# Performance work log

Hardware: AMD Instinct MI355X
Metric: run time of the kernel (lower is better)

Reference implementation:

```python
import jax, jax.numpy as jnp
import numpy as np

B, S, H = 2, 2048, 1024
NH, HD = 16, 64  # num heads, head dim
EPS = 1e-12


def setup_inputs() -> dict:
    key = jax.random.key(0)
    ks = jax.random.split(key, 10)
    sc = 1.0 / np.sqrt(H)
    return {
        "hidden_states": jax.random.normal(ks[0], (B, S, H), jnp.float32),
        "Wq": jax.random.normal(ks[1], (H, H), jnp.float32) * sc,
        "bq": jnp.zeros((H,), jnp.float32),
        "Wk": jax.random.normal(ks[2], (H, H), jnp.float32) * sc,
        "bk": jnp.zeros((H,), jnp.float32),
        "Wv": jax.random.normal(ks[3], (H, H), jnp.float32) * sc,
        "bv": jnp.zeros((H,), jnp.float32),
        "Wo": jax.random.normal(ks[4], (H, H), jnp.float32) * sc,
        "bo": jnp.zeros((H,), jnp.float32),
        "ln_g": jnp.ones((H,), jnp.float32),
        "ln_b": jnp.zeros((H,), jnp.float32),
    }


def reference(hidden_states, Wq, bq, Wk, bk, Wv, bv, Wo, bo, ln_g, ln_b):
    x = hidden_states  # [B,S,H]
    def split_heads(t):
        return t.reshape(B, S, NH, HD).transpose(0, 2, 1, 3)  # [B,NH,S,HD]
    q = split_heads(x @ Wq.T + bq)
    k = split_heads(x @ Wk.T + bk)
    v = split_heads(x @ Wv.T + bv)
    scores = jnp.einsum("bhqd,bhkd->bhqk", q, k) / np.sqrt(HD)
    causal = jnp.tril(jnp.ones((S, S), bool))  # [S,S]
    scores = jnp.where(causal[None, None], scores, -jnp.inf)
    probs = jax.nn.softmax(scores, axis=-1)
    ctx = jnp.einsum("bhqk,bhkd->bhqd", probs, v)
    ctx = ctx.transpose(0, 2, 1, 3).reshape(B, S, H)
    attn_out = ctx @ Wo.T + bo
    y = attn_out + x
    mu = jnp.mean(y, axis=-1, keepdims=True)
    var = jnp.mean((y - mu) ** 2, axis=-1, keepdims=True)
    return (y - mu) / jnp.sqrt(var + EPS) * ln_g + ln_b
```

## Files before the change

### kernel.cpp

```cpp
#include <hip/hip_runtime.h>

#define B_  2
#define S_  2048
#define H_  1024
#define NH_ 16
#define HD_ 64
#define M_  (B_*S_)

typedef __attribute__((ext_vector_type(8))) __bf16 bf16x8;
typedef __attribute__((ext_vector_type(4))) float  f32x4;
typedef __attribute__((ext_vector_type(8))) unsigned short us8;
typedef __attribute__((ext_vector_type(4))) float  fl4;

__device__ __forceinline__ unsigned short f2bf(float f) {
    unsigned int u = __float_as_uint(f);
    u += 0x7fffu + ((u >> 16) & 1u);
    return (unsigned short)(u >> 16);
}

__global__ __launch_bounds__(256) void cast_kernel(
    const float* __restrict__ x,
    const float* __restrict__ wq, const float* __restrict__ wk,
    const float* __restrict__ wv, const float* __restrict__ wo,
    unsigned short* __restrict__ xb, unsigned short* __restrict__ wb) {
    size_t t  = (size_t)blockIdx.x * 256 + threadIdx.x;
    size_t e0 = t * 4;
    const size_t XN = (size_t)M_ * H_;
    const float* src;
    unsigned short* dst;
    if (e0 < XN) { src = x + e0; dst = xb + e0; }
    else {
        size_t j = e0 - XN;
        int w = (int)(j >> 20);
        size_t off = j & ((1u << 20) - 1);
        const float* wp = (w == 0) ? wq : (w == 1) ? wk : (w == 2) ? wv : wo;
        src = wp + off; dst = wb + j;
    }
    fl4 v = *(const fl4*)src;
    ushort4 o;
    o.x = f2bf(v.x); o.y = f2bf(v.y); o.z = f2bf(v.z); o.w = f2bf(v.w);
    *(ushort4*)dst = o;
}

__global__ __launch_bounds__(512) void gemm_qkv(
    const unsigned short* __restrict__ xb, const unsigned short* __restrict__ wb,
    const float* __restrict__ bq, const float* __restrict__ bk,
    const float* __restrict__ bv,
    unsigned short* __restrict__ qb, unsigned short* __restrict__ kbuf,
    unsigned short* __restrict__ vT) {
    __shared__ __align__(16) unsigned short As[128 * 72];
    __shared__ __align__(16) unsigned short Bs[128 * 72];
    const int z = blockIdx.z;
    const unsigned short* W = wb + ((size_t)z << 20);
    const int m0 = blockIdx.x * 128, n0 = blockIdx.y * 128;
    const int t = threadIdx.x, lane = t & 63, w = t >> 6;
    const int wm = w >> 2, wn = w & 3;
    const int quad = lane >> 4, l16 = lane & 15;
    const int sr = t >> 2, sc = (t & 3) * 16;
    const unsigned short* ga = xb + (size_t)(m0 + sr) * H_ + sc;
    const unsigned short* gb = W  + (size_t)(n0 + sr) * H_ + sc;

    us8 a0 = *(const us8*)(ga),     a1 = *(const us8*)(ga + 8);
    us8 b0 = *(const us8*)(gb),     b1 = *(const us8*)(gb + 8);

    f32x4 acc[4][2] = {};
    for (int k0 = 0; k0 < H_; k0 += 64) {
        if (k0) __syncthreads();
        *(us8*)&As[sr * 72 + sc]     = a0;  *(us8*)&As[sr * 72 + sc + 8] = a1;
        *(us8*)&Bs[sr * 72 + sc]     = b0;  *(us8*)&Bs[sr * 72 + sc + 8] = b1;
        __syncthreads();
        if (k0 + 64 < H_) {
            ga += 64; gb += 64;
            a0 = *(const us8*)(ga);  a1 = *(const us8*)(ga + 8);
            b0 = *(const us8*)(gb);  b1 = *(const us8*)(gb + 8);
        }
#pragma unroll
        for (int kk = 0; kk < 64; kk += 32) {
            bf16x8 af[4], bfr[2];
#pragma unroll
            for (int i = 0; i < 4; i++)
                af[i]  = *(const bf16x8*)&As[(wm * 64 + i * 16 + l16) * 72 + kk + quad * 8];
#pragma unroll
            for (int jn = 0; jn < 2; jn++)
                bfr[jn] = *(const bf16x8*)&Bs[(wn * 32 + jn * 16 + l16) * 72 + kk + quad * 8];
#pragma unroll
            for (int mi = 0; mi < 4; mi++)
#pragma unroll
                for (int ni = 0; ni < 2; ni++)
                    acc[mi][ni] = __builtin_amdgcn_mfma_f32_16x16x32_bf16(
                        af[mi], bfr[ni], acc[mi][ni], 0, 0, 0);
        }
    }
    const float* bias = (z == 0) ? bq : (z == 1) ? bk : bv;
    if (z == 2) {
#pragma unroll
        for (int mi = 0; mi < 4; mi++) {
#pragma unroll
            for (int ni = 0; ni < 2; ni++) {
                int col  = n0 + wn * 32 + ni * 16 + l16;
                float bval = bias[col];
                int row0 = m0 + wm * 64 + mi * 16 + quad * 4;
                int bb = row0 >> 11, s0 = row0 & 2047;
                ushort4 pk;
                pk.x = f2bf(acc[mi][ni][0] + bval);
                pk.y = f2bf(acc[mi][ni][1] + bval);
                pk.z = f2bf(acc[mi][ni][2] + bval);
                pk.w = f2bf(acc[mi][ni][3] + bval);
                *(ushort4*)&vT[((size_t)bb * NH_ * HD_ + col) * S_ + s0] = pk;
            }
        }
    } else {
        unsigned short* out = (z == 0) ? qb : kbuf;
        const float qs = (z == 0) ? 0.18033688f : 1.0f;
#pragma unroll
        for (int mi = 0; mi < 4; mi++) {
#pragma unroll
            for (int ni = 0; ni < 2; ni++) {
                int col = n0 + wn * 32 + ni * 16 + l16;
                float bval = bias[col];
#pragma unroll
                for (int r = 0; r < 4; r++) {
                    int row = m0 + wm * 64 + mi * 16 + quad * 4 + r;
                    out[(size_t)row * H_ + col] = f2bf((acc[mi][ni][r] + bval) * qs);
                }
            }
        }
    }
}

__global__ __launch_bounds__(512) void gemm_out(
    const unsigned short* __restrict__ ctxb, const unsigned short* __restrict__ wob,
    const float* __restrict__ bo, const float* __restrict__ x,
    float* __restrict__ y) {
    __shared__ __align__(16) unsigned short As[128 * 72];
    __shared__ __align__(16) unsigned short Bs[128 * 72];
    const int m0 = blockIdx.x * 128, n0 = blockIdx.y * 128;
    const int t = threadIdx.x, lane = t & 63, w = t >> 6;
    const int wm = w >> 2, wn = w & 3;
    const int quad = lane >> 4, l16 = lane & 15;
    const int sr = t >> 2, sc = (t & 3) * 16;
    const unsigned short* ga = ctxb + (size_t)(m0 + sr) * H_ + sc;
    const unsigned short* gb = wob  + (size_t)(n0 + sr) * H_ + sc;

    us8 a0 = *(const us8*)(ga),     a1 = *(const us8*)(ga + 8);
    us8 b0 = *(const us8*)(gb),     b1 = *(const us8*)(gb + 8);

    f32x4 acc[4][2] = {};
    for (int k0 = 0; k0 < H_; k0 += 64) {
        if (k0) __syncthreads();
        *(us8*)&As[sr * 72 + sc]     = a0;  *(us8*)&As[sr * 72 + sc + 8] = a1;
        *(us8*)&Bs[sr * 72 + sc]     = b0;  *(us8*)&Bs[sr * 72 + sc + 8] = b1;
        __syncthreads();
        if (k0 + 64 < H_) {
            ga += 64; gb += 64;
            a0 = *(const us8*)(ga);  a1 = *(const us8*)(ga + 8);
            b0 = *(const us8*)(gb);  b1 = *(const us8*)(gb + 8);
        }
#pragma unroll
        for (int kk = 0; kk < 64; kk += 32) {
            bf16x8 af[4], bfr[2];
#pragma unroll
            for (int i = 0; i < 4; i++)
                af[i]  = *(const bf16x8*)&As[(wm * 64 + i * 16 + l16) * 72 + kk + quad * 8];
#pragma unroll
            for (int jn = 0; jn < 2; jn++)
                bfr[jn] = *(const bf16x8*)&Bs[(wn * 32 + jn * 16 + l16) * 72 + kk + quad * 8];
#pragma unroll
            for (int mi = 0; mi < 4; mi++)
#pragma unroll
                for (int ni = 0; ni < 2; ni++)
                    acc[mi][ni] = __builtin_amdgcn_mfma_f32_16x16x32_bf16(
                        af[mi], bfr[ni], acc[mi][ni], 0, 0, 0);
        }
    }
#pragma unroll
    for (int mi = 0; mi < 4; mi++) {
#pragma unroll
        for (int ni = 0; ni < 2; ni++) {
            int col = n0 + wn * 32 + ni * 16 + l16;
            float bval = bo[col];
#pragma unroll
            for (int r = 0; r < 4; r++) {
                size_t idx = (size_t)(m0 + wm * 64 + mi * 16 + quad * 4 + r) * H_ + col;
                y[idx] = acc[mi][ni][r] + bval + x[idx];
            }
        }
    }
}

__global__ __launch_bounds__(512, 4) void attn_kernel(
    const unsigned short* __restrict__ qb, const unsigned short* __restrict__ kb,
    const unsigned short* __restrict__ vT, unsigned short* __restrict__ ctxb) {
    __shared__ __align__(16) unsigned short Ks[2][64 * 72];
    __shared__ __align__(16) unsigned short Vt[2][64 * 72];
    __shared__ __align__(16) unsigned short Ps[128 * 76];
    const int flat = blockIdx.x;
    const int xcd = flat & 7, slot = flat >> 3;
    const int bh  = xcd * 4 + (slot >> 3);
    const int j   = slot & 7;
    const int b = bh >> 4, h = bh & 15;
    const int t = threadIdx.x, lane = t & 63, wid = t >> 6;
    const int grp = wid >> 2, wid4 = wid & 3;
    const int quad = lane >> 4, l16 = lane & 15;
    const int sr8 = t >> 3, sc8 = (t & 7) * 8;
    const size_t headoff = (size_t)h * HD_;
    const unsigned short* vtb = vT + ((size_t)(b * NH_ + h) * HD_) * S_;

    const int p   = j * 2 + grp;
    const int qt1 = p, qt2 = 31 - p;
    const int q01 = qt1 * 64, q02 = qt2 * 64;

    const size_t qr1 = (size_t)(b * S_ + q01 + wid4 * 16 + l16);
    const size_t qr2 = (size_t)(b * S_ + q02 + wid4 * 16 + l16);
    bf16x8 q1a = *(const bf16x8*)(qb + qr1 * H_ + headoff + quad * 8);
    bf16x8 q1b = *(const bf16x8*)(qb + qr1 * H_ + headoff + 32 + quad * 8);
    bf16x8 q2a = *(const bf16x8*)(qb + qr2 * H_ + headoff + quad * 8);
    bf16x8 q2b = *(const bf16x8*)(qb + qr2 * H_ + headoff + 32 + quad * 8);

    float m1 = -1e30f, l1 = 0.f, m2 = -1e30f, l2 = 0.f;
    f32x4 o1[4] = {}, o2[4] = {};

    const unsigned short* kptr = kb  + (size_t)(b * S_ + sr8) * H_ + headoff + sc8;
    const unsigned short* vptr = vtb + (size_t)sr8 * S_ + sc8;
    us8 nk = *(const us8*)kptr;
    us8 nv = *(const us8*)vptr;
    *(us8*)&Ks[0][sr8 * 72 + sc8] = nk;
    *(us8*)&Vt[0][sr8 * 72 + sc8] = nv;
    __syncthreads();

    for (int s = 0; s < 32; s++) {
        const int buf = s & 1;
        const bool pf = (s < 31);
        if (pf) {
            kptr += (size_t)64 * H_;
            vptr += 64;
            nk = *(const us8*)kptr;
            nv = *(const us8*)vptr;
        }
#pragma unroll
        for (int tile = 0; tile < 2; tile++) {
            const int  qt  = tile ? qt2 : qt1;
            if (s > qt) continue;
            const bf16x8 qa = tile ? q2a : q1a;
            const bf16x8 qb_ = tile ? q2b : q1b;
            f32x4 sacc[4] = {};
#pragma unroll
            for (int kk = 0; kk < 64; kk += 32) {
                bf16x8 bqf = (kk == 0) ? qa : qb_;
#pragma unroll
                for (int nt = 0; nt < 4; nt++) {
                    bf16x8 ak = *(const bf16x8*)&Ks[buf][(nt * 16 + l16) * 72 + kk + quad * 8];
                    sacc[nt] = __builtin_amdgcn_mfma_f32_16x16x32_bf16(ak, bqf, sacc[nt], 0, 0, 0);
                }
            }
            if (s == qt) {
#pragma unroll
                for (int nt = 0; nt < 4; nt++) {
#pragma unroll
                    for (int r = 0; r < 4; r++) {
                        int key = nt * 16 + quad * 4 + r;
                        if (key > wid4 * 16 + l16) sacc[nt][r] = -1e30f;
                    }
                }
            }
            float mx = sacc[0][0];
#pragma unroll
            for (int nt = 0; nt < 4; nt++)
#pragma unroll
                for (int r = 0; r < 4; r++) mx = fmaxf(mx, sacc[nt][r]);
            mx = fmaxf(mx, __shfl_xor(mx, 16));
            mx = fmaxf(mx, __shfl_xor(mx, 32));
            float m_old = tile ? m2 : m1;
            float m_new = fmaxf(m_old, mx);
            float alpha = exp2f(m_old - m_new);
            float ss = 0.f;
#pragma unroll
            for (int nt = 0; nt < 4; nt++) {
                ushort4 pk;
                float p0 = exp2f(sacc[nt][0] - m_new);
                float p1 = exp2f(sacc[nt][1] - m_new);
                float p2 = exp2f(sacc[nt][2] - m_new);
                float p3 = exp2f(sacc[nt][3] - m_new);
                ss += (p0 + p1) + (p2 + p3);
                pk.x = (unsigned short)(__float_as_uint(p0) >> 16);
                pk.y = (unsigned short)(__float_as_uint(p1) >> 16);
                pk.z = (unsigned short)(__float_as_uint(p2) >> 16);
                pk.w = (unsigned short)(__float_as_uint(p3) >> 16);
                *(ushort4*)&Ps[(wid * 16 + l16) * 76 + nt * 16 + quad * 4] = pk;
            }
            ss += __shfl_xor(ss, 16);
            ss += __shfl_xor(ss, 32);
            if (tile) { l2 = l2 * alpha + ss; m2 = m_new; }
            else      { l1 = l1 * alpha + ss; m1 = m_new; }
            f32x4* oo = tile ? o2 : o1;
#pragma unroll
            for (int dt = 0; dt < 4; dt++)
#pragma unroll
                for (int r = 0; r < 4; r++) oo[dt][r] *= alpha;
            __threadfence_block();
#pragma unroll
            for (int kk = 0; kk < 64; kk += 32) {
                bf16x8 pfr = *(const bf16x8*)&Ps[(wid * 16 + l16) * 76 + kk + quad * 8];
#pragma unroll
                for (int dt = 0; dt < 4; dt++) {
                    bf16x8 vf = *(const bf16x8*)&Vt[buf][(dt * 16 + l16) * 72 + kk + quad * 8];
                    oo[dt] = __builtin_amdgcn_mfma_f32_16x16x32_bf16(vf, pfr, oo[dt], 0, 0, 0);
                }
            }
        }
        if (pf) {
            *(us8*)&Ks[buf ^ 1][sr8 * 72 + sc8] = nk;
            *(us8*)&Vt[buf ^ 1][sr8 * 72 + sc8] = nv;
            __syncthreads();
        }
    }
#pragma unroll
    for (int tile = 0; tile < 2; tile++) {
        const int q0 = tile ? q02 : q01;
        const float inv = 1.0f / (tile ? l2 : l1);
        const f32x4* oo = tile ? o2 : o1;
        size_t row = (size_t)(b * S_ + q0 + wid4 * 16 + l16);
#pragma unroll
        for (int dt = 0; dt < 4; dt++) {
            ushort4 pk;
            pk.x = f2bf(oo[dt][0] * inv);
            pk.y = f2bf(oo[dt][1] * inv);
            pk.z = f2bf(oo[dt][2] * inv);
            pk.w = f2bf(oo[dt][3] * inv);
            *(ushort4*)&ctxb[row * H_ + headoff + dt * 16 + quad * 4] = pk;
        }
    }
}

__global__ __launch_bounds__(256) void ln_kernel(
    const float* __restrict__ y, const float* __restrict__ g,
    const float* __restrict__ bta, float* __restrict__ out) {
    __shared__ float red[8];
    const int row = blockIdx.x, t = threadIdx.x;
    fl4 v = *(const fl4*)(y + (size_t)row * H_ + t * 4);
    float s  = v.x + v.y + v.z + v.w;
    float sq = v.x * v.x + v.y * v.y + v.z * v.z + v.w * v.w;
    for (int m = 1; m < 64; m <<= 1) { s += __shfl_xor(s, m); sq += __shfl_xor(sq, m); }
    const int wid = t >> 6, lane = t & 63;
    if (lane == 0) { red[wid * 2] = s; red[wid * 2 + 1] = sq; }
    __syncthreads();
    s  = red[0] + red[2] + red[4] + red[6];
    sq = red[1] + red[3] + red[5] + red[7];
    float mu   = s * (1.0f / H_);
    float var  = sq * (1.0f / H_) - mu * mu;
    float rstd = rsqrtf(fmaxf(var, 0.f) + 1e-12f);
    fl4 gg = *(const fl4*)(g + t * 4);
    fl4 bb = *(const fl4*)(bta + t * 4);
    fl4 o;
    o.x = (v.x - mu) * rstd * gg.x + bb.x;
    o.y = (v.y - mu) * rstd * gg.y + bb.y;
    o.z = (v.z - mu) * rstd * gg.z + bb.z;
    o.w = (v.w - mu) * rstd * gg.w + bb.w;
    *(fl4*)(out + (size_t)row * H_ + t * 4) = o;
}

extern "C" void kernel_launch(void* const* d_in, const int* in_sizes, int n_in,
                              void* d_out, int out_size, void* d_ws, size_t ws_size,
                              hipStream_t stream) {
    const float* x  = (const float*)d_in[0];
    const float* Wq = (const float*)d_in[1];
    const float* bq = (const float*)d_in[2];
    const float* Wk = (const float*)d_in[3];
    const float* bk = (const float*)d_in[4];
    const float* Wv = (const float*)d_in[5];
    const float* bv = (const float*)d_in[6];
    const float* Wo = (const float*)d_in[7];
    const float* bo = (const float*)d_in[8];
    const float* lg = (const float*)d_in[9];
    const float* lb = (const float*)d_in[10];
    float* out = (float*)d_out;

    const size_t MEG = 1024u * 1024u;
    unsigned short* ws16 = (unsigned short*)d_ws;
    unsigned short* xb   = ws16;
    unsigned short* wb   = ws16 + 4 * MEG;
    unsigned short* qb   = ws16 + 8 * MEG;
    unsigned short* kb   = ws16 + 12 * MEG;
    unsigned short* vT   = ws16 + 16 * MEG;
    unsigned short* ctxb = ws16 + 20 * MEG;
    float* y = (float*)(ws16 + 24 * MEG);

    cast_kernel<<<8192, 256, 0, stream>>>(x, Wq, Wk, Wv, Wo, xb, wb);
    gemm_qkv<<<dim3(32, 8, 3), 512, 0, stream>>>(xb, wb, bq, bk, bv, qb, kb, vT);
    attn_kernel<<<dim3(256), 512, 0, stream>>>(qb, kb, vT, ctxb);
    gemm_out<<<dim3(32, 8), 512, 0, stream>>>(ctxb, wb + 3 * MEG, bo, x, y);
    ln_kernel<<<4096, 256, 0, stream>>>(y, lg, lb, out);
}
```

Measured before the change: 200.3 us.

## Split attention into one-query-tile blocks with causal-length loops and balanced scheduling

The attention kernel now launches 1024 blocks of 256 threads, each handling a single 64-row query tile. Previously 256 blocks of 512 threads each carried two paired query tiles and always looped over all 32 key tiles. Each block now loops only up to its causal diagonal. Block order alternates long and short tiles across rounds on each XCD to balance load. This gives more, smaller blocks for finer scheduling, but each K/V tile is now loaded once per query tile instead of being shared by two.

New measurement: 212.7 us. +6.2%, slower.

```diff
diff --git a/kernel.cpp b/kernel.cpp
--- a/kernel.cpp
+++ b/kernel.cpp
@@ -188,145 +188,133 @@
     }
 }
 
-__global__ __launch_bounds__(512, 4) void attn_kernel(
+__global__ __launch_bounds__(256) void attn_kernel(
     const unsigned short* __restrict__ qb, const unsigned short* __restrict__ kb,
     const unsigned short* __restrict__ vT, unsigned short* __restrict__ ctxb) {
     __shared__ __align__(16) unsigned short Ks[2][64 * 72];
     __shared__ __align__(16) unsigned short Vt[2][64 * 72];
-    __shared__ __align__(16) unsigned short Ps[128 * 76];
+    __shared__ __align__(16) unsigned short Ps[64 * 76];
     const int flat = blockIdx.x;
     const int xcd = flat & 7, slot = flat >> 3;
-    const int bh  = xcd * 4 + (slot >> 3);
-    const int j   = slot & 7;
+    const int round = slot >> 5, i = slot & 31;
+    const int qt = (round == 0 || round == 3) ? (31 - i) : i;
+    const int bh = xcd * 4 + round;
     const int b = bh >> 4, h = bh & 15;
     const int t = threadIdx.x, lane = t & 63, wid = t >> 6;
-    const int grp = wid >> 2, wid4 = wid & 3;
     const int quad = lane >> 4, l16 = lane & 15;
-    const int sr8 = t >> 3, sc8 = (t & 7) * 8;
+    const int sr = t >> 2, sc = (t & 3) * 16;
     const size_t headoff = (size_t)h * HD_;
     const unsigned short* vtb = vT + ((size_t)(b * NH_ + h) * HD_) * S_;
-
-    const int p   = j * 2 + grp;
-    const int qt1 = p, qt2 = 31 - p;
-    const int q01 = qt1 * 64, q02 = qt2 * 64;
-
-    const size_t qr1 = (size_t)(b * S_ + q01 + wid4 * 16 + l16);
-    const size_t qr2 = (size_t)(b * S_ + q02 + wid4 * 16 + l16);
-    bf16x8 q1a = *(const bf16x8*)(qb + qr1 * H_ + headoff + quad * 8);
-    bf16x8 q1b = *(const bf16x8*)(qb + qr1 * H_ + headoff + 32 + quad * 8);
-    bf16x8 q2a = *(const bf16x8*)(qb + qr2 * H_ + headoff + quad * 8);
-    bf16x8 q2b = *(const bf16x8*)(qb + qr2 * H_ + headoff + 32 + quad * 8);
-
-    float m1 = -1e30f, l1 = 0.f, m2 = -1e30f, l2 = 0.f;
-    f32x4 o1[4] = {}, o2[4] = {};
-
-    const unsigned short* kptr = kb  + (size_t)(b * S_ + sr8) * H_ + headoff + sc8;
-    const unsigned short* vptr = vtb + (size_t)sr8 * S_ + sc8;
-    us8 nk = *(const us8*)kptr;
-    us8 nv = *(const us8*)vptr;
-    *(us8*)&Ks[0][sr8 * 72 + sc8] = nk;
-    *(us8*)&Vt[0][sr8 * 72 + sc8] = nv;
+    const int q0 = qt * 64;
+
+    const size_t qrow = (size_t)(b * S_ + q0 + wid * 16 + l16);
+    bf16x8 qf0 = *(const bf16x8*)(qb + qrow * H_ + headoff + quad * 8);
+    bf16x8 qf1 = *(const bf16x8*)(qb + qrow * H_ + headoff + 32 + quad * 8);
+
+    float m_r = -1e30f, l_r = 0.f;
+    f32x4 o_acc[4] = {};
+
+    const unsigned short* kptr = kb  + (size_t)(b * S_ + sr) * H_ + headoff + sc;
+    const unsigned short* vptr = vtb + (size_t)sr * S_ + sc;
+    us8 nk0 = *(const us8*)(kptr);
+    us8 nk1 = *(const us8*)(kptr + 8);
+    us8 nv0 = *(const us8*)(vptr);
+    us8 nv1 = *(const us8*)(vptr + 8);
+    *(us8*)&Ks[0][sr * 72 + sc]     = nk0;  *(us8*)&Ks[0][sr * 72 + sc + 8] = nk1;
+    *(us8*)&Vt[0][sr * 72 + sc]     = nv0;  *(us8*)&Vt[0][sr * 72 + sc + 8] = nv1;
     __syncthreads();
 
-    for (int s = 0; s < 32; s++) {
+    for (int s = 0; s <= qt; s++) {
         const int buf = s & 1;
-        const bool pf = (s < 31);
+        const bool pf = (s < qt);
         if (pf) {
             kptr += (size_t)64 * H_;
             vptr += 64;
-            nk = *(const us8*)kptr;
-            nv = *(const us8*)vptr;
-        }
-#pragma unroll
-        for (int tile = 0; tile < 2; tile++) {
-            const int  qt  = tile ? qt2 : qt1;
-            if (s > qt) continue;
-            const bf16x8 qa = tile ? q2a : q1a;
-            const bf16x8 qb_ = tile ? q2b : q1b;
-            f32x4 sacc[4] = {};
-#pragma unroll
-            for (int kk = 0; kk < 64; kk += 32) {
-                bf16x8 bqf = (kk == 0) ? qa : qb_;
-#pragma unroll
-                for (int nt = 0; nt < 4; nt++) {
-                    bf16x8 ak = *(const bf16x8*)&Ks[buf][(nt * 16 + l16) * 72 + kk + quad * 8];
-                    sacc[nt] = __builtin_amdgcn_mfma_f32_16x16x32_bf16(ak, bqf, sacc[nt], 0, 0, 0);
+            nk0 = *(const us8*)(kptr);
+            nk1 = *(const us8*)(kptr + 8);
+            nv0 = *(const us8*)(vptr);
+            nv1 = *(const us8*)(vptr + 8);
+        }
+        f32x4 sacc[4] = {};
+#pragma unroll
+        for (int kk = 0; kk < 64; kk += 32) {
+            bf16x8 bq_ = (kk == 0) ? qf0 : qf1;
+#pragma unroll
+            for (int nt = 0; nt < 4; nt++) {
+                bf16x8 ak = *(const bf16x8*)&Ks[buf][(nt * 16 + l16) * 72 + kk + quad * 8];
+                sacc[nt] = __builtin_amdgcn_mfma_f32_16x16x32_bf16(ak, bq_, sacc[nt], 0, 0, 0);
+            }
+        }
+        if (s == qt) {
+#pragma unroll
+            for (int nt = 0; nt < 4; nt++) {
+#pragma unroll
+                for (int r = 0; r < 4; r++) {
+                    int key = nt * 16 + quad * 4 + r;
+                    if (key > wid * 16 + l16) sacc[nt][r] = -1e30f;
                 }
             }
-            if (s == qt) {
-#pragma unroll
-                for (int nt = 0; nt < 4; nt++) {
-#pragma unroll
-                    for (int r = 0; r < 4; r++) {
-                        int key = nt * 16 + quad * 4 + r;
-                        if (key > wid4 * 16 + l16) sacc[nt][r] = -1e30f;
-                    }
-                }
-            }
-            float mx = sacc[0][0];
-#pragma unroll
-            for (int nt = 0; nt < 4; nt++)
-#pragma unroll
-                for (int r = 0; r < 4; r++) mx = fmaxf(mx, sacc[nt][r]);
-            mx = fmaxf(mx, __shfl_xor(mx, 16));
-            mx = fmaxf(mx, __shfl_xor(mx, 32));
-            float m_old = tile ? m2 : m1;
-            float m_new = fmaxf(m_old, mx);
-            float alpha = exp2f(m_old - m_new);
-            float ss = 0.f;
-#pragma unroll
-            for (int nt = 0; nt < 4; nt++) {
-                ushort4 pk;
-                float p0 = exp2f(sacc[nt][0] - m_new);
-                float p1 = exp2f(sacc[nt][1] - m_new);
-                float p2 = exp2f(sacc[nt][2] - m_new);
-                float p3 = exp2f(sacc[nt][3] - m_new);
-                ss += (p0 + p1) + (p2 + p3);
-                pk.x = (unsigned short)(__float_as_uint(p0) >> 16);
-                pk.y = (unsigned short)(__float_as_uint(p1) >> 16);
-                pk.z = (unsigned short)(__float_as_uint(p2) >> 16);
-                pk.w = (unsigned short)(__float_as_uint(p3) >> 16);
-                *(ushort4*)&Ps[(wid * 16 + l16) * 76 + nt * 16 + quad * 4] = pk;
-            }
-            ss += __shfl_xor(ss, 16);
-            ss += __shfl_xor(ss, 32);
-            if (tile) { l2 = l2 * alpha + ss; m2 = m_new; }
-            else      { l1 = l1 * alpha + ss; m1 = m_new; }
-            f32x4* oo = tile ? o2 : o1;
-#pragma unroll
-            for (int dt = 0; dt < 4; dt++)
-#pragma unroll
-                for (int r = 0; r < 4; r++) oo[dt][r] *= alpha;
-            __threadfence_block();
-#pragma unroll
-            for (int kk = 0; kk < 64; kk += 32) {
-                bf16x8 pfr = *(const bf16x8*)&Ps[(wid * 16 + l16) * 76 + kk + quad * 8];
-#pragma unroll
-                for (int dt = 0; dt < 4; dt++) {
-                    bf16x8 vf = *(const bf16x8*)&Vt[buf][(dt * 16 + l16) * 72 + kk + quad * 8];
-                    oo[dt] = __builtin_amdgcn_mfma_f32_16x16x32_bf16(vf, pfr, oo[dt], 0, 0, 0);
-                }
+        }
+        float mx = sacc[0][0];
+#pragma unroll
+        for (int nt = 0; nt < 4; nt++)
+#pragma unroll
+            for (int r = 0; r < 4; r++) mx = fmaxf(mx, sacc[nt][r]);
+        mx = fmaxf(mx, __shfl_xor(mx, 16));
+        mx = fmaxf(mx, __shfl_xor(mx, 32));
+        float m_new = fmaxf(m_r, mx);
+        float alpha = exp2f(m_r - m_new);
+        float ss = 0.f;
+#pragma unroll
+        for (int nt = 0; nt < 4; nt++) {
+            ushort4 pk;
+            float p0 = exp2f(sacc[nt][0] - m_new);
+            float p1 = exp2f(sacc[nt][1] - m_new);
+            float p2 = exp2f(sacc[nt][2] - m_new);
+            float p3 = exp2f(sacc[nt][3] - m_new);
+            ss += (p0 + p1) + (p2 + p3);
+            pk.x = (unsigned short)(__float_as_uint(p0) >> 16);
+            pk.y = (unsigned short)(__float_as_uint(p1) >> 16);
+            pk.z = (unsigned short)(__float_as_uint(p2) >> 16);
+            pk.w = (unsigned short)(__float_as_uint(p3) >> 16);
+            *(ushort4*)&Ps[(wid * 16 + l16) * 76 + nt * 16 + quad * 4] = pk;
+        }
+        ss += __shfl_xor(ss, 16);
+        ss += __shfl_xor(ss, 32);
+        l_r = l_r * alpha + ss;
+        m_r = m_new;
+#pragma unroll
+        for (int dt = 0; dt < 4; dt++)
+#pragma unroll
+            for (int r = 0; r < 4; r++) o_acc[dt][r] *= alpha;
+        __threadfence_block();
+#pragma unroll
+        for (int kk = 0; kk < 64; kk += 32) {
+            bf16x8 pfr = *(const bf16x8*)&Ps[(wid * 16 + l16) * 76 + kk + quad * 8];
+#pragma unroll
+            for (int dt = 0; dt < 4; dt++) {
+                bf16x8 vf = *(const bf16x8*)&Vt[buf][(dt * 16 + l16) * 72 + kk + quad * 8];
+                o_acc[dt] = __builtin_amdgcn_mfma_f32_16x16x32_bf16(vf, pfr, o_acc[dt], 0, 0, 0);
             }
         }
         if (pf) {
-            *(us8*)&Ks[buf ^ 1][sr8 * 72 + sc8] = nk;
-            *(us8*)&Vt[buf ^ 1][sr8 * 72 + sc8] = nv;
+            *(us8*)&Ks[buf ^ 1][sr * 72 + sc]     = nk0;
+            *(us8*)&Ks[buf ^ 1][sr * 72 + sc + 8] = nk1;
+            *(us8*)&Vt[buf ^ 1][sr * 72 + sc]     = nv0;
+            *(us8*)&Vt[buf ^ 1][sr * 72 + sc + 8] = nv1;
             __syncthreads();
         }
     }
-#pragma unroll
-    for (int tile = 0; tile < 2; tile++) {
-        const int q0 = tile ? q02 : q01;
-        const float inv = 1.0f / (tile ? l2 : l1);
-        const f32x4* oo = tile ? o2 : o1;
-        size_t row = (size_t)(b * S_ + q0 + wid4 * 16 + l16);
+    {
+        float inv = 1.0f / l_r;
+        size_t row = (size_t)(b * S_ + q0 + wid * 16 + l16);
 #pragma unroll
         for (int dt = 0; dt < 4; dt++) {
             ushort4 pk;
-            pk.x = f2bf(oo[dt][0] * inv);
-            pk.y = f2bf(oo[dt][1] * inv);
-            pk.z = f2bf(oo[dt][2] * inv);
-            pk.w = f2bf(oo[dt][3] * inv);
+            pk.x = f2bf(o_acc[dt][0] * inv);
+            pk.y = f2bf(o_acc[dt][1] * inv);
+            pk.z = f2bf(o_acc[dt][2] * inv);
+            pk.w = f2bf(o_acc[dt][3] * inv);
             *(ushort4*)&ctxb[row * H_ + headoff + dt * 16 + quad * 4] = pk;
         }
     }
@@ -387,7 +375,7 @@
 
     cast_kernel<<<8192, 256, 0, stream>>>(x, Wq, Wk, Wv, Wo, xb, wb);
     gemm_qkv<<<dim3(32, 8, 3), 512, 0, stream>>>(xb, wb, bq, bk, bv, qb, kb, vT);
-    attn_kernel<<<dim3(256), 512, 0, stream>>>(qb, kb, vT, ctxb);
+    attn_kernel<<<dim3(1024), 256, 0, stream>>>(qb, kb, vT, ctxb);
     gemm_out<<<dim3(32, 8), 512, 0, stream>>>(ctxb, wb + 3 * MEG, bo, x, y);
     ln_kernel<<<4096, 256, 0, stream>>>(y, lg, lb, out);
 }
```
